# Kernel optimization log

Hardware: AMD Instinct MI355X
Metric: run time of the kernel (lower is better)

The kernel has to match this reference:

```python
import jax, jax.numpy as jnp
import numpy as np

B, NUM, LQ, LP, H = 8, 4, 128, 512, 512


def setup_inputs() -> dict:
    key = jax.random.key(0)
    k1, k2, k3 = jax.random.split(key, 3)
    return {
        "encode_input1": jax.random.normal(k1, (B, NUM, LQ, H), jnp.float32),
        "encode_input2": jax.random.normal(k2, (B, NUM, LP, H), jnp.float32),
        "input1_mask": jnp.ones((B, NUM, LQ), jnp.int32),
        "input2_mask": jnp.ones((B, NUM, LP), jnp.int32),
        "w": jax.random.normal(k3, (3 * H,), jnp.float32) * (1.0 / np.sqrt(3 * H)),
    }


def reference(encode_input1, encode_input2, input1_mask, input2_mask, w):
    Bb, num_q, Lq, Hh = encode_input1.shape
    _, num_p, Lp, _ = encode_input2.shape
    # num_q == num_p path of the original module
    E_q = encode_input1.reshape(-1, Lq, Hh)            # [BM, Lq, H]
    E_p = encode_input2.reshape(-1, Lp, Hh)            # [BM, Lp, H]
    m_q = input1_mask.reshape(-1, Lq)
    m_p = input2_mask.reshape(-1, Lp)
    # Linear([E_q, E_p, E_q*E_p]) -> scalar decomposes into three terms;
    # avoids materializing the O(Lp*Lq*3H) broadcast-concat tensor.
    w_q, w_p, w_m = w[:Hh], w[Hh:2 * Hh], w[2 * Hh:]
    U = ((E_p @ w_p)[:, :, None]
         + (E_q @ w_q)[:, None, :]
         + jnp.einsum('bph,h,bqh->bpq', E_p, w_m, E_q))   # [BM, Lp, Lq]
    mask = (m_p[:, :, None] * m_q[:, None, :]).astype(bool)
    Um = jnp.where(mask, U, jnp.finfo(U.dtype).min)
    A_p = jnp.where(mask, jax.nn.softmax(Um, axis=2), 0.0)   # row softmax over Lq
    B_p = jnp.where(mask, jax.nn.softmax(Um, axis=1), 0.0)   # col softmax over Lp
    A1 = A_p @ E_q                                   # [BM, Lp, H]
    B1 = jnp.einsum('bpq,bph->bqh', B_p, E_p)        # [BM, Lq, H]
    A2 = A_p @ B1                                    # [BM, Lp, H]
    B2 = jnp.einsum('bpq,bph->bqh', B_p, A1)         # [BM, Lq, H]
    shp_p = (Bb, num_p, Lp, Hh)
    shp_q = (Bb, num_p, Lq, Hh)
    E_p4 = E_p.reshape(shp_p); E_q4 = E_q.reshape(shp_q)
    A1 = A1.reshape(shp_p); A2 = A2.reshape(shp_p)
    B1 = B1.reshape(shp_q); B2 = B2.reshape(shp_q)
    G_q_p = jnp.concatenate([E_p4, A1, A2, E_p4 * A1, E_p4 * A2], axis=-1)
    G_p_q = jnp.concatenate([E_q4, B1, B2, E_q4 * B1, E_q4 * B2], axis=-1)
    G_p_q = G_p_q * input1_mask[..., None].astype(G_p_q.dtype)
    G_q_p = G_q_p * input2_mask[..., None].astype(G_q_p.dtype)
    return (G_p_q, G_q_p)
```

## Files before the change

### kernel.cpp

```cpp
#include <hip/hip_runtime.h>
#include <hip/hip_bf16.h>

#define BBATCH 32
#define LQ 128
#define LP 512
#define HDIM 512
#define GDIM 2560
#define NEG_MAX (-3.402823466e38f)

typedef __attribute__((ext_vector_type(8))) short short8;
typedef __attribute__((ext_vector_type(4))) float f32x4;
typedef __attribute__((ext_vector_type(4))) unsigned short ushort4v;

__device__ inline unsigned short f2bf(float f) {
  union { float f; unsigned int u; } v; v.f = f;
  unsigned int r = v.u + 0x7FFFu + ((v.u >> 16) & 1u);
  return (unsigned short)(r >> 16);
}
__device__ inline float bf2f(unsigned short s) {
  union { unsigned int u; float f; } v; v.u = (unsigned int)s << 16;
  return v.f;
}

__device__ inline void stage128x64(const unsigned short* __restrict__ src, int ld,
                                   int row0, int k0, unsigned short* lds, int t) {
#pragma unroll
  for (int i = 0; i < 4; i++) {
    int o = (t + i * 256) * 16;
    int row = o >> 7, col = (o & 127) >> 1;
    int swz = o ^ ((row & 7) << 4);
    *(short8*)((char*)lds + swz) = *(const short8*)(src + (long)(row0 + row) * ld + k0 + col);
  }
}
__device__ inline void stage64x64(const unsigned short* __restrict__ src, int ld,
                                  int row0, int k0, unsigned short* lds, int t) {
#pragma unroll
  for (int i = 0; i < 2; i++) {
    int o = (t + i * 256) * 16;
    int row = o >> 7, col = (o & 127) >> 1;
    int swz = o ^ ((row & 7) << 4);
    *(short8*)((char*)lds + swz) = *(const short8*)(src + (long)(row0 + row) * ld + k0 + col);
  }
}
__device__ inline short8 fragld(const unsigned short* lds, int row, int ks, int fq) {
  return *(const short8*)((const char*)lds + (((row << 7) + ks * 64 + fq * 16) ^ ((row & 7) << 4)));
}

__global__ __launch_bounds__(256) void cast2_kernel(
    const float* __restrict__ Ep, const float* __restrict__ Eq,
    const float* __restrict__ w,
    unsigned short* __restrict__ Epb, unsigned short* __restrict__ EpT,
    unsigned short* __restrict__ Eqb, unsigned short* __restrict__ EqT,
    unsigned short* __restrict__ Eqw,
    float* __restrict__ epv, float* __restrict__ eqv) {
  const int b = blockIdx.y;
  const int bx = blockIdx.x;
  const bool isP = bx < 8;
  const int R = isP ? LP : LQ;
  const int p0 = (isP ? bx : bx - 8) * 64;
  const float* src = isP ? Ep + (long)b * LP * HDIM : Eq + (long)b * LQ * HDIM;
  const float* wb_base = isP ? w + HDIM : w;
  unsigned short* dN = isP ? Epb + (long)b * LP * HDIM : Eqb + (long)b * LQ * HDIM;
  unsigned short* dT = isP ? EpT + (long)b * HDIM * LP : EqT + (long)b * HDIM * LQ;
  unsigned short* dW = isP ? nullptr : Eqw + (long)b * LQ * HDIM;
  float* bias = (isP ? epv + b * LP : eqv + b * LQ) + p0;
  __shared__ float T[64][65];
  const int t = threadIdx.x, c4 = (t & 15) * 4, r = t >> 4;
  float dot[4] = {0.f, 0.f, 0.f, 0.f};
  for (int h0 = 0; h0 < HDIM; h0 += 64) {
    float4 wb = *(const float4*)(wb_base + h0 + c4);
    float4 wm4 = {0, 0, 0, 0};
    if (!isP) wm4 = *(const float4*)(w + 2 * HDIM + h0 + c4);
    __syncthreads();
#pragma unroll
    for (int i = 0; i < 4; i++) {
      int row = r + 16 * i;
      float4 v = *(const float4*)(src + (long)(p0 + row) * HDIM + h0 + c4);
      T[row][c4] = v.x; T[row][c4 + 1] = v.y; T[row][c4 + 2] = v.z; T[row][c4 + 3] = v.w;
      ushort4v o = {f2bf(v.x), f2bf(v.y), f2bf(v.z), f2bf(v.w)};
      *(ushort4v*)(dN + (long)(p0 + row) * HDIM + h0 + c4) = o;
      if (!isP) {
        ushort4v ow = {f2bf(v.x * wm4.x), f2bf(v.y * wm4.y), f2bf(v.z * wm4.z), f2bf(v.w * wm4.w)};
        *(ushort4v*)(dW + (long)(p0 + row) * HDIM + h0 + c4) = ow;
      }
      dot[i] += v.x * wb.x + v.y * wb.y + v.z * wb.z + v.w * wb.w;
    }
    __syncthreads();
#pragma unroll
    for (int i = 0; i < 4; i++) {
      int hh = r + 16 * i;
      ushort4v o = {f2bf(T[c4][hh]), f2bf(T[c4 + 1][hh]), f2bf(T[c4 + 2][hh]), f2bf(T[c4 + 3][hh])};
      *(ushort4v*)(dT + (long)(h0 + hh) * R + p0 + c4) = o;
    }
  }
#pragma unroll
  for (int i = 0; i < 4; i++) {
#pragma unroll
    for (int s = 1; s < 16; s <<= 1) dot[i] += __shfl_xor(dot[i], s);
  }
  if ((t & 15) == 0) {
#pragma unroll
    for (int i = 0; i < 4; i++) bias[r + 16 * i] = dot[i];
  }
}

__global__ __launch_bounds__(256) void u_gemm(
    const unsigned short* __restrict__ Ab, const unsigned short* __restrict__ Bb,
    const float* __restrict__ epv, const float* __restrict__ eqv,
    const int* __restrict__ maskM, const int* __restrict__ maskN,
    float* __restrict__ UmT, unsigned short* __restrict__ Apb) {
  const int hw = blockIdx.x;
  const int xcd = hw & 7, s_ = hw >> 3;
  const int b = xcd * 4 + (s_ >> 3);
  const int m0 = (s_ & 7) * 64;
  const unsigned short* A = Ab + (long)b * LP * HDIM;
  const unsigned short* B = Bb + (long)b * LQ * HDIM;
  __shared__ unsigned short As[4096];
  __shared__ unsigned short Bs[8192];
  __shared__ float smax[2][64], ssum[2][64];
  const int t = threadIdx.x, lane = t & 63, wid = t >> 6;
  const int wm = wid >> 1, wn = wid & 1;
  const int wr = wm * 32, wc = wn * 64;
  const int fr = lane & 15, fq = lane >> 4;
  f32x4 acc[2][4] = {};
  for (int k0 = 0; k0 < HDIM; k0 += 64) {
    stage64x64(A, HDIM, m0, k0, As, t);
    stage128x64(B, HDIM, 0, k0, Bs, t);
    __syncthreads();
#pragma unroll
    for (int ks = 0; ks < 2; ks++) {
      short8 af[2], bfv[4];
#pragma unroll
      for (int i = 0; i < 2; i++) af[i] = fragld(As, wr + i * 16 + fr, ks, fq);
#pragma unroll
      for (int j = 0; j < 4; j++) bfv[j] = fragld(Bs, wc + j * 16 + fr, ks, fq);
#pragma unroll
      for (int i = 0; i < 2; i++)
#pragma unroll
        for (int j = 0; j < 4; j++)
          acc[i][j] = __builtin_amdgcn_mfma_f32_16x16x32_bf16(af[i], bfv[j], acc[i][j], 0, 0, 0);
    }
    __syncthreads();
  }
  const float* ep_b = epv + (long)b * LP;
  const float* eq_b = eqv + (long)b * LQ;
  const int* mM = maskM + (long)b * LP;
  const int* mN = maskN + (long)b * LQ;
  float* UmTB = UmT + (long)b * LQ * LP;
  unsigned short* ApB = Apb + (long)b * LP * LQ;
  float eqc[4]; int mnc[4];
#pragma unroll
  for (int j = 0; j < 4; j++) {
    int col = wc + j * 16 + fr;
    eqc[j] = eq_b[col]; mnc[j] = mN[col];
  }
  float epr[2][4]; int mmr[2][4];
#pragma unroll
  for (int i = 0; i < 2; i++)
#pragma unroll
    for (int r = 0; r < 4; r++) {
      int row = m0 + wr + i * 16 + fq * 4 + r;
      epr[i][r] = ep_b[row]; mmr[i][r] = mM[row];
    }
#pragma unroll
  for (int i = 0; i < 2; i++)
#pragma unroll
    for (int j = 0; j < 4; j++) {
      float4 tv;
#pragma unroll
      for (int r = 0; r < 4; r++) {
        float a = acc[i][j][r];
        bool ok = mmr[i][r] && mnc[j];
        ((float*)&tv)[r] = ok ? a + epr[i][r] : NEG_MAX;
        acc[i][j][r] = ok ? a + eqc[j] : NEG_MAX;
      }
      int col = wc + j * 16 + fr;
      *(float4*)(UmTB + (long)col * LP + m0 + wr + i * 16 + fq * 4) = tv;
    }
  float mx[2][4];
#pragma unroll
  for (int i = 0; i < 2; i++)
#pragma unroll
    for (int r = 0; r < 4; r++) {
      float m = fmaxf(fmaxf(acc[i][0][r], acc[i][1][r]), fmaxf(acc[i][2][r], acc[i][3][r]));
#pragma unroll
      for (int s = 1; s < 16; s <<= 1) m = fmaxf(m, __shfl_xor(m, s));
      mx[i][r] = m;
      if (fr == 0) smax[wn][wr + i * 16 + fq * 4 + r] = m;
    }
  __syncthreads();
#pragma unroll
  for (int i = 0; i < 2; i++)
#pragma unroll
    for (int r = 0; r < 4; r++) {
      int rl = wr + i * 16 + fq * 4 + r;
      mx[i][r] = fmaxf(smax[0][rl], smax[1][rl]);
    }
#pragma unroll
  for (int i = 0; i < 2; i++)
#pragma unroll
    for (int r = 0; r < 4; r++) {
      float s = 0.f;
#pragma unroll
      for (int j = 0; j < 4; j++) {
        float e = __expf(acc[i][j][r] - mx[i][r]);
        acc[i][j][r] = e; s += e;
      }
#pragma unroll
      for (int sh = 1; sh < 16; sh <<= 1) s += __shfl_xor(s, sh);
      if (fr == 0) ssum[wn][wr + i * 16 + fq * 4 + r] = s;
    }
  __syncthreads();
#pragma unroll
  for (int i = 0; i < 2; i++)
#pragma unroll
    for (int r = 0; r < 4; r++) {
      int rl = wr + i * 16 + fq * 4 + r;
      float S = ssum[0][rl] + ssum[1][rl];
      float inv = S > 0.f ? 1.f / S : 0.f;
      int row = m0 + rl;
#pragma unroll
      for (int j = 0; j < 4; j++) {
        int col = wc + j * 16 + fr;
        bool ok = mmr[i][r] && mnc[j];
        ApB[(long)row * LQ + col] = ok ? f2bf(acc[i][j][r] * inv) : 0;
      }
    }
}

__global__ __launch_bounds__(256) void colsoftmaxT_kernel(
    const float* __restrict__ UmT, unsigned short* __restrict__ BpT,
    const int* __restrict__ mp, const int* __restrict__ mq) {
  int wid = blockIdx.x * 4 + (threadIdx.x >> 6);
  int lane = threadIdx.x & 63;
  int b = wid >> 7;
  const float* row = UmT + (long)wid * LP;
  float v[8];
  float m = NEG_MAX;
#pragma unroll
  for (int i = 0; i < 8; i++) { v[i] = row[lane + 64 * i]; m = fmaxf(m, v[i]); }
#pragma unroll
  for (int off = 32; off; off >>= 1) m = fmaxf(m, __shfl_xor(m, off));
  float e[8];
  float s = 0.f;
#pragma unroll
  for (int i = 0; i < 8; i++) { e[i] = __expf(v[i] - m); s += e[i]; }
#pragma unroll
  for (int off = 32; off; off >>= 1) s += __shfl_xor(s, off);
  float inv = s > 0.f ? 1.f / s : 0.f;
  int mqv = mq[wid];
#pragma unroll
  for (int i = 0; i < 8; i++) {
    int p = lane + 64 * i;
    bool ok = mqv && mp[b * LP + p];
    BpT[(long)wid * LP + p] = ok ? f2bf(e[i] * inv) : 0;
  }
}

template <int PHASE>
__global__ __launch_bounds__(256) void gemm_phase(
    const unsigned short* __restrict__ Apb, const unsigned short* __restrict__ BpT,
    const unsigned short* __restrict__ BA, const unsigned short* __restrict__ BB,
    const unsigned short* __restrict__ Epb, const unsigned short* __restrict__ Eqb,
    const int* __restrict__ mp, const int* __restrict__ mq,
    float* __restrict__ out_gqp, float* __restrict__ out_gpq,
    unsigned short* __restrict__ A1T, unsigned short* __restrict__ B1T) {
  const int hw = blockIdx.x;
  const int xcd = hw & 7, s_ = hw >> 3;
  const int b = xcd * 4 + (s_ / 20);
  const int bx = s_ % 20;
  __shared__ unsigned short As[8192], Bs[8192];
  const int t = threadIdx.x, lane = t & 63, wid = t >> 6;
  const int wr = (wid >> 1) * 64, wc = (wid & 1) * 64;
  const int fr = lane & 15, fq = lane >> 4;
  const unsigned short* A; const unsigned short* Bop;
  int K, M, m0, n0;
  float* outBase; const unsigned short* Eb; const int* mb;
  unsigned short* Tout;
  if (bx < 4) {
    A = BpT + (long)b * LQ * LP; K = LP; M = LQ; m0 = 0; n0 = bx * 128;
    Bop = BB + (long)b * HDIM * LP;
    outBase = out_gpq + (long)b * LQ * GDIM;
    Eb = Eqb + (long)b * LQ * HDIM; mb = mq + (long)b * LQ;
    Tout = (PHASE == 1) ? B1T + (long)b * HDIM * LQ : nullptr;
  } else {
    int idx = bx - 4; m0 = (idx >> 2) * 128; n0 = (idx & 3) * 128;
    A = Apb + (long)b * LP * LQ; K = LQ; M = LP;
    Bop = BA + (long)b * HDIM * LQ;
    outBase = out_gqp + (long)b * LP * GDIM;
    Eb = Epb + (long)b * LP * HDIM; mb = mp + (long)b * LP;
    Tout = (PHASE == 1) ? A1T + (long)b * HDIM * LP : nullptr;
  }
  f32x4 acc[4][4] = {};
  for (int k0 = 0; k0 < K; k0 += 64) {
    stage128x64(A, K, m0, k0, As, t);
    stage128x64(Bop, K, n0, k0, Bs, t);
    __syncthreads();
#pragma unroll
    for (int ks = 0; ks < 2; ks++) {
      short8 af[4], bfv[4];
#pragma unroll
      for (int i = 0; i < 4; i++) {
        af[i] = fragld(As, wr + i * 16 + fr, ks, fq);
        bfv[i] = fragld(Bs, wc + i * 16 + fr, ks, fq);
      }
#pragma unroll
      for (int i = 0; i < 4; i++)
#pragma unroll
        for (int j = 0; j < 4; j++)
          acc[i][j] = __builtin_amdgcn_mfma_f32_16x16x32_bf16(af[i], bfv[j], acc[i][j], 0, 0, 0);
    }
    __syncthreads();
  }
#pragma unroll
  for (int i = 0; i < 4; i++) {
#pragma unroll
    for (int r = 0; r < 4; r++) {
      int row = m0 + wr + i * 16 + fq * 4 + r;
      float mm = (float)mb[row];
      float* orow = outBase + (long)row * GDIM;
      const unsigned short* erow = Eb + (long)row * HDIM;
#pragma unroll
      for (int j = 0; j < 4; j++) {
        int col = n0 + wc + j * 16 + fr;
        float v = acc[i][j][r];
        float e = bf2f(erow[col]);
        if (PHASE == 1) {
          __builtin_nontemporal_store(e * mm, orow + col);
          __builtin_nontemporal_store(v * mm, orow + HDIM + col);
          __builtin_nontemporal_store(e * v * mm, orow + 3 * HDIM + col);
        } else {
          __builtin_nontemporal_store(v * mm, orow + 2 * HDIM + col);
          __builtin_nontemporal_store(e * v * mm, orow + 4 * HDIM + col);
        }
      }
    }
    if (PHASE == 1) {
#pragma unroll
      for (int j = 0; j < 4; j++) {
        int col = n0 + wc + j * 16 + fr;
        int row0 = m0 + wr + i * 16 + fq * 4;
        ushort4v o = {f2bf(acc[i][j][0]), f2bf(acc[i][j][1]),
                      f2bf(acc[i][j][2]), f2bf(acc[i][j][3])};
        *(ushort4v*)(Tout + (long)col * M + row0) = o;
      }
    }
  }
}

extern "C" void kernel_launch(void* const* d_in, const int* in_sizes, int n_in,
                              void* d_out, int out_size, void* d_ws, size_t ws_size,
                              hipStream_t stream) {
  const float* Eq = (const float*)d_in[0];
  const float* Ep = (const float*)d_in[1];
  const int* mq = (const int*)d_in[2];
  const int* mp = (const int*)d_in[3];
  const float* w = (const float*)d_in[4];
  float* out = (float*)d_out;
  float* out_gpq = out;
  float* out_gqp = out + (long)BBATCH * LQ * GDIM;

  unsigned short* Epb = (unsigned short*)d_ws;
  unsigned short* EpT = Epb + 32L * 512 * 512;
  unsigned short* Eqb = EpT + 32L * 512 * 512;
  unsigned short* EqT = Eqb + 32L * 128 * 512;
  unsigned short* Eqw = EqT + 32L * 512 * 128;
  unsigned short* Apb = Eqw + 32L * 128 * 512;
  unsigned short* BpT = Apb + 32L * 512 * 128;
  unsigned short* B1T = BpT + 32L * 128 * 512;
  unsigned short* A1T = B1T + 32L * 512 * 128;
  float* UmT = (float*)(A1T + 32L * 512 * 512);
  float* epb = UmT + 32L * 128 * 512;
  float* eqb2 = epb + 32L * 512;

  cast2_kernel<<<dim3(10, BBATCH), 256, 0, stream>>>(
      Ep, Eq, w, Epb, EpT, Eqb, EqT, Eqw, epb, eqb2);

  u_gemm<<<dim3(256), 256, 0, stream>>>(
      Epb, Eqw, epb, eqb2, mp, mq, UmT, Apb);

  colsoftmaxT_kernel<<<BBATCH * LQ / 4, 256, 0, stream>>>(UmT, BpT, mp, mq);

  gemm_phase<1><<<dim3(640), 256, 0, stream>>>(
      Apb, BpT, EqT, EpT, Epb, Eqb, mp, mq, out_gqp, out_gpq, A1T, B1T);

  gemm_phase<2><<<dim3(640), 256, 0, stream>>>(
      Apb, BpT, B1T, A1T, Epb, Eqb, mp, mq, out_gqp, out_gpq, nullptr, nullptr);
}
```

Measured before the change: 116.9 us.

## Drop bf16 copies of inputs and stage epilogue through LDS for vector stores

The prep kernel no longer writes row-major bf16 copies of Ep and Eq. The U GEMM now converts fp32 Ep to bf16 while staging into LDS, and the phase GEMMs read the original fp32 inputs for the elementwise terms. The phase GEMM epilogue now transposes accumulators through a shared-memory tile so each thread writes coalesced 16-byte nontemporal stores instead of scattered scalar stores. This cuts workspace writes and output store transactions, at the cost of reading fp32 twice as wide and extra barriers in the epilogue.

```diff
diff --git a/kernel.cpp b/kernel.cpp
--- a/kernel.cpp
+++ b/kernel.cpp
@@ -32,25 +32,29 @@
     *(short8*)((char*)lds + swz) = *(const short8*)(src + (long)(row0 + row) * ld + k0 + col);
   }
 }
-__device__ inline void stage64x64(const unsigned short* __restrict__ src, int ld,
-                                  int row0, int k0, unsigned short* lds, int t) {
+__device__ inline void stage64x64_f32(const float* __restrict__ src, int ld,
+                                      int row0, int k0, unsigned short* lds, int t) {
 #pragma unroll
   for (int i = 0; i < 2; i++) {
     int o = (t + i * 256) * 16;
     int row = o >> 7, col = (o & 127) >> 1;
     int swz = o ^ ((row & 7) << 4);
-    *(short8*)((char*)lds + swz) = *(const short8*)(src + (long)(row0 + row) * ld + k0 + col);
+    const float* p = src + (long)(row0 + row) * ld + k0 + col;
+    float4 a = *(const float4*)p;
+    float4 b2 = *(const float4*)(p + 4);
+    short8 v = {(short)f2bf(a.x), (short)f2bf(a.y), (short)f2bf(a.z), (short)f2bf(a.w),
+                (short)f2bf(b2.x), (short)f2bf(b2.y), (short)f2bf(b2.z), (short)f2bf(b2.w)};
+    *(short8*)((char*)lds + swz) = v;
   }
 }
 __device__ inline short8 fragld(const unsigned short* lds, int row, int ks, int fq) {
   return *(const short8*)((const char*)lds + (((row << 7) + ks * 64 + fq * 16) ^ ((row & 7) << 4)));
 }
 
-__global__ __launch_bounds__(256) void cast2_kernel(
+__global__ __launch_bounds__(256) void prep_kernel(
     const float* __restrict__ Ep, const float* __restrict__ Eq,
     const float* __restrict__ w,
-    unsigned short* __restrict__ Epb, unsigned short* __restrict__ EpT,
-    unsigned short* __restrict__ Eqb, unsigned short* __restrict__ EqT,
+    unsigned short* __restrict__ EpT, unsigned short* __restrict__ EqT,
     unsigned short* __restrict__ Eqw,
     float* __restrict__ epv, float* __restrict__ eqv) {
   const int b = blockIdx.y;
@@ -60,7 +64,6 @@
   const int p0 = (isP ? bx : bx - 8) * 64;
   const float* src = isP ? Ep + (long)b * LP * HDIM : Eq + (long)b * LQ * HDIM;
   const float* wb_base = isP ? w + HDIM : w;
-  unsigned short* dN = isP ? Epb + (long)b * LP * HDIM : Eqb + (long)b * LQ * HDIM;
   unsigned short* dT = isP ? EpT + (long)b * HDIM * LP : EqT + (long)b * HDIM * LQ;
   unsigned short* dW = isP ? nullptr : Eqw + (long)b * LQ * HDIM;
   float* bias = (isP ? epv + b * LP : eqv + b * LQ) + p0;
@@ -77,8 +80,6 @@
       int row = r + 16 * i;
       float4 v = *(const float4*)(src + (long)(p0 + row) * HDIM + h0 + c4);
       T[row][c4] = v.x; T[row][c4 + 1] = v.y; T[row][c4 + 2] = v.z; T[row][c4 + 3] = v.w;
-      ushort4v o = {f2bf(v.x), f2bf(v.y), f2bf(v.z), f2bf(v.w)};
-      *(ushort4v*)(dN + (long)(p0 + row) * HDIM + h0 + c4) = o;
       if (!isP) {
         ushort4v ow = {f2bf(v.x * wm4.x), f2bf(v.y * wm4.y), f2bf(v.z * wm4.z), f2bf(v.w * wm4.w)};
         *(ushort4v*)(dW + (long)(p0 + row) * HDIM + h0 + c4) = ow;
@@ -105,7 +106,7 @@
 }
 
 __global__ __launch_bounds__(256) void u_gemm(
-    const unsigned short* __restrict__ Ab, const unsigned short* __restrict__ Bb,
+    const float* __restrict__ EpF, const unsigned short* __restrict__ Bb,
     const float* __restrict__ epv, const float* __restrict__ eqv,
     const int* __restrict__ maskM, const int* __restrict__ maskN,
     float* __restrict__ UmT, unsigned short* __restrict__ Apb) {
@@ -113,7 +114,7 @@
   const int xcd = hw & 7, s_ = hw >> 3;
   const int b = xcd * 4 + (s_ >> 3);
   const int m0 = (s_ & 7) * 64;
-  const unsigned short* A = Ab + (long)b * LP * HDIM;
+  const float* A = EpF + (long)b * LP * HDIM;
   const unsigned short* B = Bb + (long)b * LQ * HDIM;
   __shared__ unsigned short As[4096];
   __shared__ unsigned short Bs[8192];
@@ -124,7 +125,7 @@
   const int fr = lane & 15, fq = lane >> 4;
   f32x4 acc[2][4] = {};
   for (int k0 = 0; k0 < HDIM; k0 += 64) {
-    stage64x64(A, HDIM, m0, k0, As, t);
+    stage64x64_f32(A, HDIM, m0, k0, As, t);
     stage128x64(B, HDIM, 0, k0, Bs, t);
     __syncthreads();
 #pragma unroll
@@ -261,7 +262,7 @@
 __global__ __launch_bounds__(256) void gemm_phase(
     const unsigned short* __restrict__ Apb, const unsigned short* __restrict__ BpT,
     const unsigned short* __restrict__ BA, const unsigned short* __restrict__ BB,
-    const unsigned short* __restrict__ Epb, const unsigned short* __restrict__ Eqb,
+    const float* __restrict__ EpF, const float* __restrict__ EqF,
     const int* __restrict__ mp, const int* __restrict__ mq,
     float* __restrict__ out_gqp, float* __restrict__ out_gpq,
     unsigned short* __restrict__ A1T, unsigned short* __restrict__ B1T) {
@@ -269,26 +270,29 @@
   const int xcd = hw & 7, s_ = hw >> 3;
   const int b = xcd * 4 + (s_ / 20);
   const int bx = s_ % 20;
-  __shared__ unsigned short As[8192], Bs[8192];
+  __shared__ __align__(16) char smem[32768];
+  unsigned short* As = (unsigned short*)smem;
+  unsigned short* Bs = (unsigned short*)(smem + 16384);
+  float (*Cs)[132] = (float(*)[132])smem;
   const int t = threadIdx.x, lane = t & 63, wid = t >> 6;
   const int wr = (wid >> 1) * 64, wc = (wid & 1) * 64;
   const int fr = lane & 15, fq = lane >> 4;
   const unsigned short* A; const unsigned short* Bop;
   int K, M, m0, n0;
-  float* outBase; const unsigned short* Eb; const int* mb;
+  float* outBase; const float* Eb; const int* mb;
   unsigned short* Tout;
   if (bx < 4) {
     A = BpT + (long)b * LQ * LP; K = LP; M = LQ; m0 = 0; n0 = bx * 128;
     Bop = BB + (long)b * HDIM * LP;
     outBase = out_gpq + (long)b * LQ * GDIM;
-    Eb = Eqb + (long)b * LQ * HDIM; mb = mq + (long)b * LQ;
+    Eb = EqF + (long)b * LQ * HDIM; mb = mq + (long)b * LQ;
     Tout = (PHASE == 1) ? B1T + (long)b * HDIM * LQ : nullptr;
   } else {
     int idx = bx - 4; m0 = (idx >> 2) * 128; n0 = (idx & 3) * 128;
     A = Apb + (long)b * LP * LQ; K = LQ; M = LP;
     Bop = BA + (long)b * HDIM * LQ;
     outBase = out_gqp + (long)b * LP * GDIM;
-    Eb = Epb + (long)b * LP * HDIM; mb = mp + (long)b * LP;
+    Eb = EpF + (long)b * LP * HDIM; mb = mp + (long)b * LP;
     Tout = (PHASE == 1) ? A1T + (long)b * HDIM * LP : nullptr;
   }
   f32x4 acc[4][4] = {};
@@ -312,30 +316,9 @@
     }
     __syncthreads();
   }
-#pragma unroll
-  for (int i = 0; i < 4; i++) {
-#pragma unroll
-    for (int r = 0; r < 4; r++) {
-      int row = m0 + wr + i * 16 + fq * 4 + r;
-      float mm = (float)mb[row];
-      float* orow = outBase + (long)row * GDIM;
-      const unsigned short* erow = Eb + (long)row * HDIM;
-#pragma unroll
-      for (int j = 0; j < 4; j++) {
-        int col = n0 + wc + j * 16 + fr;
-        float v = acc[i][j][r];
-        float e = bf2f(erow[col]);
-        if (PHASE == 1) {
-          __builtin_nontemporal_store(e * mm, orow + col);
-          __builtin_nontemporal_store(v * mm, orow + HDIM + col);
-          __builtin_nontemporal_store(e * v * mm, orow + 3 * HDIM + col);
-        } else {
-          __builtin_nontemporal_store(v * mm, orow + 2 * HDIM + col);
-          __builtin_nontemporal_store(e * v * mm, orow + 4 * HDIM + col);
-        }
-      }
-    }
-    if (PHASE == 1) {
+  if (PHASE == 1) {
+#pragma unroll
+    for (int i = 0; i < 4; i++)
 #pragma unroll
       for (int j = 0; j < 4; j++) {
         int col = n0 + wc + j * 16 + fr;
@@ -343,6 +326,39 @@
         ushort4v o = {f2bf(acc[i][j][0]), f2bf(acc[i][j][1]),
                       f2bf(acc[i][j][2]), f2bf(acc[i][j][3])};
         *(ushort4v*)(Tout + (long)col * M + row0) = o;
+      }
+  }
+  const int band = wid >> 1;
+#pragma unroll
+  for (int i = 0; i < 4; i++) {
+    __syncthreads();
+#pragma unroll
+    for (int j = 0; j < 4; j++) {
+#pragma unroll
+      for (int r = 0; r < 4; r++)
+        Cs[band * 16 + fq * 4 + r][wc + j * 16 + fr] = acc[i][j][r];
+    }
+    __syncthreads();
+#pragma unroll
+    for (int k = 0; k < 4; k++) {
+      int slot = t + k * 256;
+      int row_l = slot >> 5;
+      int c4 = (slot & 31) * 4;
+      int bnd = row_l >> 4;
+      int r_g = m0 + bnd * 64 + i * 16 + (row_l & 15);
+      float mm = (float)mb[r_g];
+      f32x4 v = *(f32x4*)&Cs[row_l][c4];
+      f32x4 e = *(const f32x4*)(Eb + (long)r_g * HDIM + n0 + c4);
+      float* orow = outBase + (long)r_g * GDIM + n0 + c4;
+      f32x4 vm = v * mm;
+      f32x4 evm = e * vm;
+      if (PHASE == 1) {
+        __builtin_nontemporal_store(e * mm, (f32x4*)(orow));
+        __builtin_nontemporal_store(vm, (f32x4*)(orow + HDIM));
+        __builtin_nontemporal_store(evm, (f32x4*)(orow + 3 * HDIM));
+      } else {
+        __builtin_nontemporal_store(vm, (f32x4*)(orow + 2 * HDIM));
+        __builtin_nontemporal_store(evm, (f32x4*)(orow + 4 * HDIM));
       }
     }
   }
@@ -360,10 +376,8 @@
   float* out_gpq = out;
   float* out_gqp = out + (long)BBATCH * LQ * GDIM;
 
-  unsigned short* Epb = (unsigned short*)d_ws;
-  unsigned short* EpT = Epb + 32L * 512 * 512;
-  unsigned short* Eqb = EpT + 32L * 512 * 512;
-  unsigned short* EqT = Eqb + 32L * 128 * 512;
+  unsigned short* EpT = (unsigned short*)d_ws;
+  unsigned short* EqT = EpT + 32L * 512 * 512;
   unsigned short* Eqw = EqT + 32L * 512 * 128;
   unsigned short* Apb = Eqw + 32L * 128 * 512;
   unsigned short* BpT = Apb + 32L * 512 * 128;
@@ -373,17 +387,17 @@
   float* epb = UmT + 32L * 128 * 512;
   float* eqb2 = epb + 32L * 512;
 
-  cast2_kernel<<<dim3(10, BBATCH), 256, 0, stream>>>(
-      Ep, Eq, w, Epb, EpT, Eqb, EqT, Eqw, epb, eqb2);
+  prep_kernel<<<dim3(10, BBATCH), 256, 0, stream>>>(
+      Ep, Eq, w, EpT, EqT, Eqw, epb, eqb2);
 
   u_gemm<<<dim3(256), 256, 0, stream>>>(
-      Epb, Eqw, epb, eqb2, mp, mq, UmT, Apb);
+      Ep, Eqw, epb, eqb2, mp, mq, UmT, Apb);
 
   colsoftmaxT_kernel<<<BBATCH * LQ / 4, 256, 0, stream>>>(UmT, BpT, mp, mq);
 
   gemm_phase<1><<<dim3(640), 256, 0, stream>>>(
-      Apb, BpT, EqT, EpT, Epb, Eqb, mp, mq, out_gqp, out_gpq, A1T, B1T);
+      Apb, BpT, EqT, EpT, Ep, Eq, mp, mq, out_gqp, out_gpq, A1T, B1T);
 
   gemm_phase<2><<<dim3(640), 256, 0, stream>>>(
-      Apb, BpT, B1T, A1T, Epb, Eqb, mp, mq, out_gqp, out_gpq, nullptr, nullptr);
-}
+      Apb, BpT, B1T, A1T, Ep, Eq, mp, mq, out_gqp, out_gpq, nullptr, nullptr);
+}
```

New measurement: 107.2 us. 8.3% less time.
